# Performance work log

Measured on AMD Instinct MI355X. Metric: run time of the kernel, lower is better.

The kernel has to match this reference:

```python
import jax, jax.numpy as jnp
import numpy as np

NF, NA, NC = 100000, 400, 30   # flight, airport, carrier node counts
N = NF + NA + NC               # total nodes after type concatenation
D = 256                        # hidden_channels
B = 3                          # num_bases
R = 4                          # num_relations
E = 250000                     # edges per relation


def setup_inputs() -> dict:
    key = jax.random.key(0)
    ks = jax.random.split(key, 32)
    inp = {
        'x_flight': jax.random.normal(ks[0], (NF, 32), jnp.float32),
        'x_airport': jax.random.normal(ks[1], (NA, 16), jnp.float32),
        'x_carrier': jax.random.normal(ks[2], (NC, 8), jnp.float32),
        # per-type encoders (Linear stored as [in, out])
        'W_f': jax.random.normal(ks[3], (32, D), jnp.float32) * 0.05,
        'b_f': jnp.zeros((D,), jnp.float32),
        'W_a': jax.random.normal(ks[4], (16, D), jnp.float32) * 0.05,
        'b_a': jnp.zeros((D,), jnp.float32),
        'W_c': jax.random.normal(ks[5], (8, D), jnp.float32) * 0.05,
        'b_c': jnp.zeros((D,), jnp.float32),
        # RGCNConv layer 0: basis decomposition W_r = sum_b comp[r,b] * basis[b]
        'basis0': jax.random.normal(ks[6], (B, D, D), jnp.float32) * 0.02,
        'comp0': jax.random.normal(ks[7], (R, B), jnp.float32) * 0.5,
        'root0': jax.random.normal(ks[8], (D, D), jnp.float32) * 0.02,
        'bias0': jnp.zeros((D,), jnp.float32),
        # RGCNConv layer 1
        'basis1': jax.random.normal(ks[9], (B, D, D), jnp.float32) * 0.02,
        'comp1': jax.random.normal(ks[10], (R, B), jnp.float32) * 0.5,
        'root1': jax.random.normal(ks[11], (D, D), jnp.float32) * 0.02,
        'bias1': jnp.zeros((D,), jnp.float32),
        # readout Linear(D -> 1)
        'W_out': jax.random.normal(ks[12], (D, 1), jnp.float32) * 0.05,
        'b_out': jnp.zeros((1,), jnp.float32),
        # per-relation edge lists (local indices within src/dst node type)
        'src0': jax.random.randint(ks[13], (E,), 0, NF),
        'dst0': jax.random.randint(ks[14], (E,), 0, NA),
        'src1': jax.random.randint(ks[15], (E,), 0, NA),
        'dst1': jax.random.randint(ks[16], (E,), 0, NF),
        'src2': jax.random.randint(ks[17], (E,), 0, NF),
        'dst2': jax.random.randint(ks[18], (E,), 0, NC),
        'src3': jax.random.randint(ks[19], (E,), 0, NC),
        'dst3': jax.random.randint(ks[20], (E,), 0, NF),
    }
    return inp


def _rgcn_conv(x, basis, comp, root, bias, edges):
    """PyG RGCNConv with basis decomposition, mean aggregation per relation."""
    W = jnp.einsum('rb,bio->rio', comp, basis)  # [R, D, D]
    out = x @ root + bias                        # root/self transform
    for r, (src, dst) in enumerate(edges):       # R=4 fixed relations
        msg = x[src] @ W[r]                                        # [E, D]
        agg = jax.ops.segment_sum(msg, dst, num_segments=N)        # [N, D]
        deg = jax.ops.segment_sum(jnp.ones((dst.shape[0],), x.dtype), dst,
                                  num_segments=N)
        out = out + agg / jnp.maximum(deg, 1.0)[:, None]           # mean aggr
    return out


def reference(x_flight, x_airport, x_carrier,
              W_f, b_f, W_a, b_a, W_c, b_c,
              basis0, comp0, root0, bias0,
              basis1, comp1, root1, bias1,
              W_out, b_out,
              src0, dst0, src1, dst1, src2, dst2, src3, dst3):
    # per-type encoders + ReLU, then concat into homogeneous node tensor
    hf = jax.nn.relu(x_flight @ W_f + b_f)
    ha = jax.nn.relu(x_airport @ W_a + b_a)
    hc = jax.nn.relu(x_carrier @ W_c + b_c)
    x = jnp.concatenate([hf, ha, hc], axis=0)  # offsets: flight=0, airport=NF, carrier=NF+NA
    edges = [
        (src0, dst0 + NF),        # flight -> airport
        (src1 + NF, dst1),        # airport -> flight
        (src2, dst2 + NF + NA),   # flight -> carrier
        (src3 + NF + NA, dst3),   # carrier -> flight
    ]
    x = jax.nn.relu(_rgcn_conv(x, basis0, comp0, root0, bias0, edges))
    x = jax.nn.relu(_rgcn_conv(x, basis1, comp1, root1, bias1, edges))
    # dropout is identity in eval mode
    return (x[:NF] @ W_out + b_out).squeeze(-1)  # [NF]
```

## Files before the change

### kernel.cpp

```cpp
#include <hip/hip_runtime.h>
#include <hip/hip_bf16.h>
#include <cstdint>
#include <cstddef>

constexpr int NF = 100000;
constexpr int NA = 400;
constexpr int NC = 30;
constexpr int NN = NF + NA + NC;
constexpr int D  = 256;
constexpr int DD = D * D;
constexpr int E  = 250000;
constexpr int NSL = 128;

typedef __attribute__((ext_vector_type(8))) short bf16x8;
typedef __attribute__((ext_vector_type(4))) float f32x4;
typedef __attribute__((ext_vector_type(8))) ushort u16x8;

__device__ inline ushort f2bf(float f) {
    __hip_bfloat16 h = __float2bfloat16(f);
    return __builtin_bit_cast(ushort, h);
}
__device__ inline float bf2f(ushort u) {
    __hip_bfloat16 h = __builtin_bit_cast(__hip_bfloat16, u);
    return __bfloat162float(h);
}

__device__ inline void gload_lds16(const ushort* g, ushort* l) {
    __builtin_amdgcn_global_load_lds(
        (const __attribute__((address_space(1))) void*)g,
        (__attribute__((address_space(3))) void*)l, 16, 0, 0);
}

template<int K, int ROWS>
__global__ __launch_bounds__(256) void encode_kernel(
    const float* __restrict__ x, const float* __restrict__ W,
    const float* __restrict__ b, ushort* __restrict__ hH,
    int rows, int row_off)
{
    int c = threadIdx.x;
    int base = blockIdx.x * ROWS;
    float wcol[K];
    #pragma unroll
    for (int k = 0; k < K; ++k) wcol[k] = W[k * D + c];
    float bias = b[c];
    for (int i = 0; i < ROWS; ++i) {
        int row = base + i;
        if (row >= rows) return;
        const float* xr = x + (size_t)row * K;
        float acc = bias;
        #pragma unroll
        for (int k = 0; k < K; ++k) acc += xr[k] * wcol[k];
        hH[(size_t)(row_off + row) * D + c] = f2bf(fmaxf(acc, 0.f));
    }
}

__global__ __launch_bounds__(256) void wsplit_kernel(
    const float* __restrict__ root, ushort* __restrict__ WtH, ushort* __restrict__ WtL)
{
    int n = blockIdx.x, k = threadIdx.x;
    float w = root[(size_t)k * D + n];
    ushort hi = f2bf(w);
    WtH[(size_t)n * D + k] = hi;
    WtL[(size_t)n * D + k] = f2bf(w - bf2f(hi));
}

__global__ __launch_bounds__(256) void wr_kernel(
    const float* __restrict__ basis, const float* __restrict__ comp,
    float* __restrict__ wr)
{
    int idx = blockIdx.x * 256 + threadIdx.x;
    int r = idx >> 16;
    int io = idx & (DD - 1);
    wr[idx] = comp[r * 3 + 0] * basis[io]
            + comp[r * 3 + 1] * basis[DD + io]
            + comp[r * 3 + 2] * basis[2 * DD + io];
}

__global__ __launch_bounds__(256) void deg_count_kernel(
    const int* __restrict__ dst1, const int* __restrict__ dst3,
    int* __restrict__ deg1, int* __restrict__ deg3)
{
    int idx = blockIdx.x * 256 + threadIdx.x;
    if (idx >= 2 * E) return;
    if (idx < E) atomicAdd(&deg1[dst1[idx]], 1);
    else         atomicAdd(&deg3[dst3[idx - E]], 1);
}

__global__ __launch_bounds__(256) void hist02_kernel(
    const int* __restrict__ dst0, const int* __restrict__ dst2,
    int* __restrict__ bh0, int* __restrict__ bh2)
{
    __shared__ int hist[NA];
    int b = blockIdx.x;
    bool isR2 = (b >= NSL);
    int sl = isR2 ? b - NSL : b;
    const int* dst = isR2 ? dst2 : dst0;
    int nb = isR2 ? NC : NA;
    for (int i = threadIdx.x; i < nb; i += 256) hist[i] = 0;
    __syncthreads();
    int lo = (int)((long long)E * sl / NSL);
    int hi = (int)((long long)E * (sl + 1) / NSL);
    for (int e = lo + threadIdx.x; e < hi; e += 256)
        atomicAdd(&hist[dst[e]], 1);
    __syncthreads();
    int* bh = isR2 ? (bh2 + sl * NC) : (bh0 + sl * NA);
    for (int i = threadIdx.x; i < nb; i += 256) bh[i] = hist[i];
}

__global__ __launch_bounds__(512) void scan02_kernel(
    int* __restrict__ bh0, int* __restrict__ bh2,
    int* __restrict__ rp0, int* __restrict__ rp2,
    float* __restrict__ inv0, float* __restrict__ inv2)
{
    __shared__ int tot[512];
    __shared__ int exc[512];
    int t = threadIdx.x;
    int cnt = 0;
    if (t < NA) {
        int s = 0;
        for (int sl = 0; sl < NSL; ++sl) {
            int v = bh0[sl * NA + t]; bh0[sl * NA + t] = s; s += v;
        }
        cnt = s;
    } else if (t < NA + NC) {
        int bin = t - NA; int s = 0;
        for (int sl = 0; sl < NSL; ++sl) {
            int v = bh2[sl * NC + bin]; bh2[sl * NC + bin] = s; s += v;
        }
        cnt = s;
    }
    tot[t] = cnt;
    __syncthreads();
    for (int ofs = 1; ofs < 512; ofs <<= 1) {
        int v = (t >= ofs) ? tot[t - ofs] : 0;
        __syncthreads();
        tot[t] += v;
        __syncthreads();
    }
    int ex = tot[t] - cnt;
    if (t < NA) {
        exc[t] = ex;
        rp0[t] = ex;
        inv0[t] = 1.0f / (float)(cnt > 1 ? cnt : 1);
        if (t == 0) { rp0[NA] = E; rp2[NC] = E; }
    } else if (t < NA + NC) {
        exc[t] = ex - E;
        rp2[t - NA] = ex - E;
        inv2[t - NA] = 1.0f / (float)(cnt > 1 ? cnt : 1);
    } else exc[t] = 0;
    __syncthreads();
    for (int idx = t; idx < NSL * NA; idx += 512) {
        int sl = idx / NA; int bin = idx - sl * NA;
        bh0[idx] += exc[bin];
    }
    for (int idx = t; idx < NSL * NC; idx += 512) {
        int sl = idx / NC; int bin = idx - sl * NC;
        bh2[idx] += exc[NA + bin];
    }
}

__global__ __launch_bounds__(256) void fill02_kernel(
    const int* __restrict__ src0, const int* __restrict__ dst0,
    const int* __restrict__ src2, const int* __restrict__ dst2,
    const int* __restrict__ bh0, const int* __restrict__ bh2,
    int* __restrict__ csr0, int* __restrict__ csr2)
{
    __shared__ int cur[NA];
    int b = blockIdx.x;
    bool isR2 = (b >= NSL);
    int sl = isR2 ? b - NSL : b;
    const int* src = isR2 ? src2 : src0;
    const int* dst = isR2 ? dst2 : dst0;
    const int* bh  = isR2 ? (bh2 + sl * NC) : (bh0 + sl * NA);
    int* csr       = isR2 ? csr2 : csr0;
    int nb = isR2 ? NC : NA;
    for (int i = threadIdx.x; i < nb; i += 256) cur[i] = bh[i];
    __syncthreads();
    int lo = (int)((long long)E * sl / NSL);
    int hi = (int)((long long)E * (sl + 1) / NSL);
    for (int e = lo + threadIdx.x; e < hi; e += 256) {
        int pos = atomicAdd(&cur[dst[e]], 1);
        csr[pos] = src[e];
    }
}

__global__ __launch_bounds__(1024) void scanA_kernel(
    const int* __restrict__ deg1, const int* __restrict__ deg3, int* __restrict__ bsum)
{
    __shared__ int s[1024];
    int b = blockIdx.x;
    bool isR3 = (b >= 98);
    const int* deg = isR3 ? deg3 : deg1;
    int chunk = isR3 ? b - 98 : b;
    int i = chunk * 1024 + threadIdx.x;
    int v = (i < NF) ? deg[i] : 0;
    s[threadIdx.x] = v;
    __syncthreads();
    for (int ofs = 512; ofs > 0; ofs >>= 1) {
        if ((int)threadIdx.x < ofs) s[threadIdx.x] += s[threadIdx.x + ofs];
        __syncthreads();
    }
    if (threadIdx.x == 0) bsum[(isR3 ? 128 : 0) + chunk] = s[0];
}

__global__ __launch_bounds__(256) void scanB_kernel(int* __restrict__ bsum)
{
    __shared__ int s[256];
    int t = threadIdx.x;
    int v = ((t & 127) < 98) ? bsum[t] : 0;
    s[t] = v;
    __syncthreads();
    for (int ofs = 1; ofs < 128; ofs <<= 1) {
        int a = ((t & 127) >= ofs) ? s[t - ofs] : 0;
        __syncthreads();
        s[t] += a;
        __syncthreads();
    }
    bsum[t] = s[t] - v;
}

__global__ __launch_bounds__(1024) void scanC_kernel(
    const int* __restrict__ deg1, const int* __restrict__ deg3,
    const int* __restrict__ bsum,
    int* __restrict__ rp1, int* __restrict__ rp3,
    int* __restrict__ cu1, int* __restrict__ cu3,
    float* __restrict__ inv1, float* __restrict__ inv3)
{
    __shared__ int s[1024];
    int b = blockIdx.x;
    const int* deg; int* rp; int* cu; float* inv; int chunk; int prefix;
    if (b < 98) { deg = deg1; rp = rp1; cu = cu1; inv = inv1; chunk = b;      prefix = bsum[chunk]; }
    else        { deg = deg3; rp = rp3; cu = cu3; inv = inv3; chunk = b - 98; prefix = bsum[128 + chunk]; }
    int tid = threadIdx.x;
    int i = chunk * 1024 + tid;
    int v = (i < NF) ? deg[i] : 0;
    s[tid] = v;
    __syncthreads();
    for (int ofs = 1; ofs < 1024; ofs <<= 1) {
        int a = (tid >= ofs) ? s[tid - ofs] : 0;
        __syncthreads();
        s[tid] += a;
        __syncthreads();
    }
    int ex = prefix + s[tid] - v;
    if (i < NF) {
        rp[i] = ex;
        cu[i] = ex;
        inv[i] = 1.0f / (float)(v > 1 ? v : 1);
    }
    if (i == 0) rp[NF] = E;
}

__global__ __launch_bounds__(256) void csr_fill13_kernel(
    const int* __restrict__ src1, const int* __restrict__ dst1,
    const int* __restrict__ src3, const int* __restrict__ dst3,
    int* __restrict__ cu1, int* __restrict__ cu3,
    int* __restrict__ csr1, int* __restrict__ csr3)
{
    int idx = blockIdx.x * 256 + threadIdx.x;
    if (idx >= 2 * E) return;
    if (idx < E) {
        int pos = atomicAdd(&cu1[dst1[idx]], 1);
        csr1[pos] = src1[idx];
    } else {
        int e = idx - E;
        int pos = atomicAdd(&cu3[dst3[e]], 1);
        csr3[pos] = src3[e];
    }
}

__global__ __launch_bounds__(256) void y_kernel(
    const ushort* __restrict__ hH, const float* __restrict__ wr,
    float* __restrict__ y)
{
    int row = blockIdx.x;
    int c = threadIdx.x;
    const ushort* sH = hH + (size_t)(NF + row) * D;
    const float* W = wr + (size_t)((row < NA) ? 1 : 3) * DD;
    float acc = 0.f;
    #pragma unroll 8
    for (int k = 0; k < D; ++k) acc += bf2f(sH[k]) * W[k * D + c];
    y[(size_t)row * D + c] = acc;
}

__global__ __launch_bounds__(512) void gemm_mfma(
    const ushort* __restrict__ A,
    const ushort* __restrict__ WtH, const ushort* __restrict__ WtL,
    const float* __restrict__ bias,
    ushort* __restrict__ G, int nrows)
{
    constexpr int BM = 128, BK = 32;
    constexpr int PLANE = BM * BK;
    constexpr int LDW = 36;
    __shared__ __align__(16) ushort lds[12288];
    const int t = threadIdx.x;
    const int row0 = blockIdx.x * BM;
    const int col0 = blockIdx.y * BM;
    const int w = t >> 6, lane = t & 63;
    const int wm = w >> 2, wn = w & 3;
    const int lr = lane & 15;
    const int lk = lane >> 4;
    f32x4 acc[4][2] = {};

    const ushort* sp[3];
    ushort* dp[3];
    #pragma unroll
    for (int i = 0; i < 3; ++i) {
        int idx = w * 3 + i;
        int plane = idx >> 3, g = idx & 7;
        const ushort* base = (plane == 0) ? A : (plane == 1) ? WtH : WtL;
        int r = ((plane == 0) ? row0 : col0) + g * 16 + lr;
        if (plane == 0 && r >= nrows) r = nrows - 1;
        sp[i] = base + (size_t)r * D + lk * 8;
        dp[i] = lds + plane * PLANE + g * 512;
    }

    for (int k0 = 0; k0 < D; k0 += BK) {
        #pragma unroll
        for (int i = 0; i < 3; ++i)
            gload_lds16(sp[i] + k0, dp[i]);
        __syncthreads();
        const ushort* As  = lds;
        const ushort* WsH = lds + PLANE;
        const ushort* WsL = lds + 2 * PLANE;
        bf16x8 bh[2], bl[2];
        #pragma unroll
        for (int ni = 0; ni < 2; ++ni) {
            int off = (wn * 2 + ni) * 512 + lane * 8;
            bh[ni] = *(const bf16x8*)(&WsH[off]);
            bl[ni] = *(const bf16x8*)(&WsL[off]);
        }
        #pragma unroll
        for (int mi = 0; mi < 4; ++mi) {
            int off = (wm * 4 + mi) * 512 + lane * 8;
            bf16x8 ah = *(const bf16x8*)(&As[off]);
            #pragma unroll
            for (int ni = 0; ni < 2; ++ni) {
                acc[mi][ni] = __builtin_amdgcn_mfma_f32_16x16x32_bf16(ah, bh[ni], acc[mi][ni], 0, 0, 0);
                acc[mi][ni] = __builtin_amdgcn_mfma_f32_16x16x32_bf16(ah, bl[ni], acc[mi][ni], 0, 0, 0);
            }
        }
        __syncthreads();
    }
    float* S = (float*)lds + (size_t)w * 16 * LDW;
    const int rrow = lane >> 2;
    const int grp  = lane & 3;
    #pragma unroll
    for (int mi = 0; mi < 4; ++mi) {
        __syncthreads();
        #pragma unroll
        for (int ni = 0; ni < 2; ++ni)
            #pragma unroll
            for (int reg = 0; reg < 4; ++reg)
                S[(lk * 4 + reg) * LDW + ni * 16 + lr] = acc[mi][ni][reg];
        __syncthreads();
        int gr = row0 + wm * 64 + mi * 16 + rrow;
        int gc = col0 + wn * 32 + grp * 8;
        if (gr >= nrows) continue;
        float4 f0 = *(const float4*)(&S[rrow * LDW + grp * 8]);
        float4 f1 = *(const float4*)(&S[rrow * LDW + grp * 8 + 4]);
        float4 b0 = *(const float4*)(bias + gc);
        float4 b1 = *(const float4*)(bias + gc + 4);
        float v[8] = {f0.x + b0.x, f0.y + b0.y, f0.z + b0.z, f0.w + b0.w,
                      f1.x + b1.x, f1.y + b1.y, f1.z + b1.z, f1.w + b1.w};
        u16x8 hh;
        #pragma unroll
        for (int j = 0; j < 8; ++j) hh[j] = f2bf(v[j]);
        *(u16x8*)(G + (size_t)gr * D + gc) = hh;
    }
}

__global__ __launch_bounds__(256) void msg_relu_kernel(
    ushort* __restrict__ G,
    const float* __restrict__ y,
    const int* __restrict__ rp1, const int* __restrict__ csr1, const float* __restrict__ inv1,
    const int* __restrict__ rp3, const int* __restrict__ csr3, const float* __restrict__ inv3)
{
    int wid = (blockIdx.x * 256 + threadIdx.x) >> 6;
    int lane = threadIdx.x & 63;
    int row = wid * 2 + (lane >> 5);
    if (row >= NF) return;
    int c = (lane & 31) * 8;
    size_t o = (size_t)row * D + c;
    u16x8 gh = *(const u16x8*)(G + o);
    float v[8];
    #pragma unroll
    for (int j = 0; j < 8; ++j) v[j] = bf2f(gh[j]);
    float m[8] = {};
    int e0 = rp1[row], e1 = rp1[row + 1];
    for (int e = e0; e < e1; ++e) {
        const float* yr = y + (size_t)csr1[e] * D + c;
        float4 u0 = *(const float4*)yr;
        float4 u1 = *(const float4*)(yr + 4);
        m[0] += u0.x; m[1] += u0.y; m[2] += u0.z; m[3] += u0.w;
        m[4] += u1.x; m[5] += u1.y; m[6] += u1.z; m[7] += u1.w;
    }
    float s1 = inv1[row];
    #pragma unroll
    for (int j = 0; j < 8; ++j) { v[j] += s1 * m[j]; m[j] = 0.f; }
    e0 = rp3[row]; e1 = rp3[row + 1];
    for (int e = e0; e < e1; ++e) {
        const float* yr = y + (size_t)(NA + csr3[e]) * D + c;
        float4 u0 = *(const float4*)yr;
        float4 u1 = *(const float4*)(yr + 4);
        m[0] += u0.x; m[1] += u0.y; m[2] += u0.z; m[3] += u0.w;
        m[4] += u1.x; m[5] += u1.y; m[6] += u1.z; m[7] += u1.w;
    }
    float s3 = inv3[row];
    u16x8 oh;
    #pragma unroll
    for (int j = 0; j < 8; ++j) oh[j] = f2bf(fmaxf(v[j] + s3 * m[j], 0.f));
    *(u16x8*)(G + o) = oh;
}

__global__ __launch_bounds__(256) void msg_readout_kernel(
    const ushort* __restrict__ G,
    const float* __restrict__ y,
    const int* __restrict__ rp1, const int* __restrict__ csr1, const float* __restrict__ inv1,
    const int* __restrict__ rp3, const int* __restrict__ csr3, const float* __restrict__ inv3,
    const float* __restrict__ wout, const float* __restrict__ bout,
    float* __restrict__ out)
{
    int wid = (blockIdx.x * 256 + threadIdx.x) >> 6;
    int lane = threadIdx.x & 63;
    int row = wid * 2 + (lane >> 5);
    if (row >= NF) return;
    int c = (lane & 31) * 8;
    size_t o = (size_t)row * D + c;
    u16x8 gh = *(const u16x8*)(G + o);
    float v[8];
    #pragma unroll
    for (int j = 0; j < 8; ++j) v[j] = bf2f(gh[j]);
    float m[8] = {};
    int e0 = rp1[row], e1 = rp1[row + 1];
    for (int e = e0; e < e1; ++e) {
        const float* yr = y + (size_t)csr1[e] * D + c;
        float4 u0 = *(const float4*)yr;
        float4 u1 = *(const float4*)(yr + 4);
        m[0] += u0.x; m[1] += u0.y; m[2] += u0.z; m[3] += u0.w;
        m[4] += u1.x; m[5] += u1.y; m[6] += u1.z; m[7] += u1.w;
    }
    float s1 = inv1[row];
    #pragma unroll
    for (int j = 0; j < 8; ++j) { v[j] += s1 * m[j]; m[j] = 0.f; }
    e0 = rp3[row]; e1 = rp3[row + 1];
    for (int e = e0; e < e1; ++e) {
        const float* yr = y + (size_t)(NA + csr3[e]) * D + c;
        float4 u0 = *(const float4*)yr;
        float4 u1 = *(const float4*)(yr + 4);
        m[0] += u0.x; m[1] += u0.y; m[2] += u0.z; m[3] += u0.w;
        m[4] += u1.x; m[5] += u1.y; m[6] += u1.z; m[7] += u1.w;
    }
    float s3 = inv3[row];
    float4 w0 = *(const float4*)(wout + c);
    float4 w1 = *(const float4*)(wout + c + 4);
    float wv[8] = {w0.x, w0.y, w0.z, w0.w, w1.x, w1.y, w1.z, w1.w};
    float pr = 0.f;
    #pragma unroll
    for (int j = 0; j < 8; ++j) pr += fmaxf(v[j] + s3 * m[j], 0.f) * wv[j];
    pr += __shfl_xor(pr, 1);
    pr += __shfl_xor(pr, 2);
    pr += __shfl_xor(pr, 4);
    pr += __shfl_xor(pr, 8);
    pr += __shfl_xor(pr, 16);
    if ((lane & 31) == 0) out[row] = pr + bout[0];
}

__global__ __launch_bounds__(256) void agg_small_kernel(
    const ushort* __restrict__ hH,
    const int* __restrict__ rp0, const int* __restrict__ csr0,
    const int* __restrict__ rp2, const int* __restrict__ csr2,
    float* __restrict__ agg)
{
    __shared__ float red[4][256];
    int b = blockIdx.x;
    const int* rp; const int* csr; int dstn, chunk, nch; float* arow;
    if (b < NA * 4) { dstn = b >> 2; chunk = b & 3; nch = 4;  rp = rp0; csr = csr0; arow = agg + (size_t)dstn * D; }
    else { int bb = b - NA * 4; dstn = bb >> 6; chunk = bb & 63; nch = 64; rp = rp2; csr = csr2; arow = agg + (size_t)(NA + dstn) * D; }
    int s = rp[dstn], e = rp[dstn + 1];
    int cnt = e - s;
    int lo = s + (int)((long long)cnt * chunk / nch);
    int hi = s + (int)((long long)cnt * (chunk + 1) / nch);
    int w = threadIdx.x >> 6, lane = threadIdx.x & 63;
    int span = hi - lo;
    int wlo = lo + (int)((long long)span * w / 4);
    int whi = lo + (int)((long long)span * (w + 1) / 4);
    int half = lane >> 5;
    int ch8 = (lane & 31) * 8;
    float acc[8] = {};
    int p = wlo;
    for (; p + 1 < whi; p += 2) {
        int r = csr[p + half];
        u16x8 v = *(const u16x8*)(hH + (size_t)r * D + ch8);
        #pragma unroll
        for (int j = 0; j < 8; ++j) acc[j] += bf2f(v[j]);
    }
    if (p < whi && half == 0) {
        int r = csr[p];
        u16x8 v = *(const u16x8*)(hH + (size_t)r * D + ch8);
        #pragma unroll
        for (int j = 0; j < 8; ++j) acc[j] += bf2f(v[j]);
    }
    #pragma unroll
    for (int j = 0; j < 8; ++j) acc[j] += __shfl_xor(acc[j], 32);
    if (lane < 32) {
        #pragma unroll
        for (int j = 0; j < 8; ++j) red[w][ch8 + j] = acc[j];
    }
    __syncthreads();
    int c = threadIdx.x;
    float total = red[0][c] + red[1][c] + red[2][c] + red[3][c];
    atomicAdd(arow + c, total);
}

__global__ __launch_bounds__(256) void smallT_kernel(
    const float* __restrict__ agg, const float* __restrict__ wr,
    const float* __restrict__ inv0, const float* __restrict__ inv2,
    ushort* __restrict__ G)
{
    int row = blockIdx.x;
    int c = threadIdx.x;
    const float* a = agg + (size_t)row * D;
    const float* W = wr + (size_t)((row < NA) ? 0 : 2) * DD;
    float scale = (row < NA) ? inv0[row] : inv2[row - NA];
    float acc = 0.f;
    #pragma unroll 8
    for (int k = 0; k < D; ++k) acc += a[k] * W[k * D + c];
    size_t o = (size_t)(NF + row) * D + c;
    G[o] = f2bf(fmaxf(bf2f(G[o]) + scale * acc, 0.f));
}

extern "C" void kernel_launch(void* const* d_in, const int* in_sizes, int n_in,
                              void* d_out, int out_size, void* d_ws, size_t ws_size,
                              hipStream_t stream)
{
    const float* xf = (const float*)d_in[0];
    const float* xa = (const float*)d_in[1];
    const float* xc = (const float*)d_in[2];
    const float* Wf = (const float*)d_in[3];
    const float* bf = (const float*)d_in[4];
    const float* Wa = (const float*)d_in[5];
    const float* ba = (const float*)d_in[6];
    const float* Wc = (const float*)d_in[7];
    const float* bc = (const float*)d_in[8];
    const float* basis0 = (const float*)d_in[9];
    const float* comp0  = (const float*)d_in[10];
    const float* root0  = (const float*)d_in[11];
    const float* bias0  = (const float*)d_in[12];
    const float* basis1 = (const float*)d_in[13];
    const float* comp1  = (const float*)d_in[14];
    const float* root1  = (const float*)d_in[15];
    const float* bias1  = (const float*)d_in[16];
    const float* Wout = (const float*)d_in[17];
    const float* bout = (const float*)d_in[18];
    const int* src0 = (const int*)d_in[19];
    const int* dst0 = (const int*)d_in[20];
    const int* src1 = (const int*)d_in[21];
    const int* dst1 = (const int*)d_in[22];
    const int* src2 = (const int*)d_in[23];
    const int* dst2 = (const int*)d_in[24];
    const int* src3 = (const int*)d_in[25];
    const int* dst3 = (const int*)d_in[26];
    float* out = (float*)d_out;

    char* ws = (char*)d_ws;
    size_t off = 0;
    auto alloc = [&](size_t bytes) -> char* {
        char* p = ws + off;
        off = (off + bytes + 255) & ~(size_t)255;
        return p;
    };
    ushort* hH  = (ushort*)alloc((size_t)NN * D * 2);
    ushort* gH  = (ushort*)alloc((size_t)NN * D * 2);
    ushort* g2H = hH;
    ushort* WtH = (ushort*)alloc((size_t)DD * 2);
    ushort* WtL = (ushort*)alloc((size_t)DD * 2);
    float* wrbuf  = (float*)alloc((size_t)4 * DD * 4);
    float* ybuf   = (float*)alloc((size_t)(NA + NC) * D * 4);
    float* aggbuf = (float*)alloc((size_t)(NA + NC) * D * 4);
    int*   deg13  = (int*)  alloc((size_t)2 * NF * 4);
    int* deg1 = deg13; int* deg3 = deg13 + NF;
    float* inv1 = (float*)alloc((size_t)NF * 4);
    float* inv3 = (float*)alloc((size_t)NF * 4);
    float* inv0 = (float*)alloc((size_t)NA * 4);
    float* inv2 = (float*)alloc((size_t)NC * 4);
    int* rp0 = (int*)alloc((NA + 1) * 4);
    int* rp1 = (int*)alloc((size_t)(NF + 1) * 4);
    int* rp2 = (int*)alloc((NC + 1) * 4);
    int* rp3 = (int*)alloc((size_t)(NF + 1) * 4);
    int* cu1 = (int*)alloc((size_t)(NF + 1) * 4);
    int* cu3 = (int*)alloc((size_t)(NF + 1) * 4);
    int* csr0 = (int*)alloc((size_t)E * 4);
    int* csr1 = (int*)alloc((size_t)E * 4);
    int* csr2 = (int*)alloc((size_t)E * 4);
    int* csr3 = (int*)alloc((size_t)E * 4);
    int* bsum = (int*)alloc(256 * 4);
    int* bh0  = (int*)alloc((size_t)NSL * NA * 4);
    int* bh2  = (int*)alloc((size_t)NSL * NC * 4);
    (void)ws_size; (void)in_sizes; (void)n_in; (void)out_size;

    hist02_kernel<<<2 * NSL, 256, 0, stream>>>(dst0, dst2, bh0, bh2);
    scan02_kernel<<<1, 512, 0, stream>>>(bh0, bh2, rp0, rp2, inv0, inv2);
    fill02_kernel<<<2 * NSL, 256, 0, stream>>>(src0, dst0, src2, dst2, bh0, bh2, csr0, csr2);

    hipMemsetAsync(deg13, 0, (size_t)2 * NF * 4, stream);
    deg_count_kernel<<<(2 * E + 255) / 256, 256, 0, stream>>>(dst1, dst3, deg1, deg3);
    scanA_kernel<<<196, 1024, 0, stream>>>(deg1, deg3, bsum);
    scanB_kernel<<<1, 256, 0, stream>>>(bsum);
    scanC_kernel<<<196, 1024, 0, stream>>>(deg1, deg3, bsum, rp1, rp3, cu1, cu3, inv1, inv3);
    csr_fill13_kernel<<<(2 * E + 255) / 256, 256, 0, stream>>>(
        src1, dst1, src3, dst3, cu1, cu3, csr1, csr3);

    encode_kernel<32, 8><<<NF / 8, 256, 0, stream>>>(xf, Wf, bf, hH, NF, 0);
    encode_kernel<16, 8><<<(NA + 7) / 8, 256, 0, stream>>>(xa, Wa, ba, hH, NA, NF);
    encode_kernel<8, 8><<<(NC + 7) / 8, 256, 0, stream>>>(xc, Wc, bc, hH, NC, NF + NA);

    wsplit_kernel<<<D, D, 0, stream>>>(root0, WtH, WtL);
    wr_kernel<<<4 * DD / 256, 256, 0, stream>>>(basis0, comp0, wrbuf);
    y_kernel<<<NA + NC, 256, 0, stream>>>(hH, wrbuf, ybuf);
    gemm_mfma<<<dim3((NN + 127) / 128, 2), 512, 0, stream>>>(
        hH, WtH, WtL, bias0, gH, NN);
    hipMemsetAsync(aggbuf, 0, (size_t)(NA + NC) * D * 4, stream);
    agg_small_kernel<<<NA * 4 + NC * 64, 256, 0, stream>>>(
        hH, rp0, csr0, rp2, csr2, aggbuf);
    smallT_kernel<<<NA + NC, 256, 0, stream>>>(aggbuf, wrbuf, inv0, inv2, gH);
    msg_relu_kernel<<<(NF / 2 * 64 + 255) / 256, 256, 0, stream>>>(
        gH, ybuf, rp1, csr1, inv1, rp3, csr3, inv3);

    wsplit_kernel<<<D, D, 0, stream>>>(root1, WtH, WtL);
    wr_kernel<<<4 * DD / 256, 256, 0, stream>>>(basis1, comp1, wrbuf);
    y_kernel<<<NA + NC, 256, 0, stream>>>(gH, wrbuf, ybuf);
    gemm_mfma<<<dim3((NF + 127) / 128, 2), 512, 0, stream>>>(
        gH, WtH, WtL, bias1, g2H, NF);
    msg_readout_kernel<<<(NF / 2 * 64 + 255) / 256, 256, 0, stream>>>(
        g2H, ybuf, rp1, csr1, inv1, rp3, csr3, inv3, Wout, bout, out);
}
```

Baseline: 406.6 us.

## Double-buffer LDS tiles in MFMA GEMM to overlap global loads with compute

Splits the GEMM K-loop into stage/compute phases over two LDS buffers, prefetching the next BK slice while MFMAs run on the current one. It replaces the two syncthreads per iteration with one vmcnt wait plus a barrier, and adds sched_barriers so the compiler keeps that order. The cost is twice the LDS per block (48KB), which may lower occupancy.

Result: no change. 402.9 us (-0.9%).

```diff
diff --git a/kernel.cpp b/kernel.cpp
--- a/kernel.cpp
+++ b/kernel.cpp
@@ -291,8 +291,9 @@
 {
     constexpr int BM = 128, BK = 32;
     constexpr int PLANE = BM * BK;
+    constexpr int BUF = 3 * PLANE;
     constexpr int LDW = 36;
-    __shared__ __align__(16) ushort lds[12288];
+    __shared__ __align__(16) ushort lds[2 * BUF];
     const int t = threadIdx.x;
     const int row0 = blockIdx.x * BM;
     const int col0 = blockIdx.y * BM;
@@ -303,7 +304,7 @@
     f32x4 acc[4][2] = {};
 
     const ushort* sp[3];
-    ushort* dp[3];
+    int dofs[3];
     #pragma unroll
     for (int i = 0; i < 3; ++i) {
         int idx = w * 3 + i;
@@ -312,17 +313,20 @@
         int r = ((plane == 0) ? row0 : col0) + g * 16 + lr;
         if (plane == 0 && r >= nrows) r = nrows - 1;
         sp[i] = base + (size_t)r * D + lk * 8;
-        dp[i] = lds + plane * PLANE + g * 512;
-    }
-
-    for (int k0 = 0; k0 < D; k0 += BK) {
+        dofs[i] = plane * PLANE + g * 512;
+    }
+
+    auto stage = [&](int k0, int buf) {
+        ushort* bb = lds + buf * BUF;
         #pragma unroll
         for (int i = 0; i < 3; ++i)
-            gload_lds16(sp[i] + k0, dp[i]);
-        __syncthreads();
-        const ushort* As  = lds;
-        const ushort* WsH = lds + PLANE;
-        const ushort* WsL = lds + 2 * PLANE;
+            gload_lds16(sp[i] + k0, bb + dofs[i]);
+    };
+    auto compute = [&](int buf) {
+        const ushort* base = lds + buf * BUF;
+        const ushort* As  = base;
+        const ushort* WsH = base + PLANE;
+        const ushort* WsL = base + 2 * PLANE;
         bf16x8 bh[2], bl[2];
         #pragma unroll
         for (int ni = 0; ni < 2; ++ni) {
@@ -340,8 +344,23 @@
                 acc[mi][ni] = __builtin_amdgcn_mfma_f32_16x16x32_bf16(ah, bl[ni], acc[mi][ni], 0, 0, 0);
             }
         }
-        __syncthreads();
-    }
+    };
+
+    stage(0, 0);
+    asm volatile("s_waitcnt vmcnt(0)" ::: "memory");
+    __builtin_amdgcn_s_barrier();
+    __builtin_amdgcn_sched_barrier(0);
+    for (int kt = 0; kt < 7; ++kt) {
+        stage((kt + 1) * BK, (kt + 1) & 1);
+        __builtin_amdgcn_sched_barrier(0);
+        compute(kt & 1);
+        asm volatile("s_waitcnt vmcnt(0)" ::: "memory");
+        __builtin_amdgcn_s_barrier();
+        __builtin_amdgcn_sched_barrier(0);
+    }
+    compute(1);
+
+    __syncthreads();
     float* S = (float*)lds + (size_t)w * 16 * LDW;
     const int rrow = lane >> 2;
     const int grp  = lane & 3;
```
